# Optimization experiments

Hardware: AMD Instinct MI355X
Metric: run time of the kernel (lower is better)

Reference implementation:

```python
import jax, jax.numpy as jnp
import numpy as np


def setup_inputs() -> dict:
    key = jax.random.key(0)
    k1, k2 = jax.random.split(key)
    x = jax.random.normal(k1, (32, 128, 64, 64), dtype=jnp.float32)
    weight = jax.random.normal(k2, (256, 128, 3, 3), dtype=jnp.float32)
    return {"x": x, "weight": weight}


def reference(x, weight):
    # Batched VALID cross-correlation, stride 1 (same math as the triple loop
    # of single-channel conv2d calls summed over in_channels).
    # x: [B, Cin, H, W]; weight: [Cout, Cin, k, k] -> out: [B, Cout, H-k+1, W-k+1]
    return jax.lax.conv_general_dilated(
        x, weight,
        window_strides=(1, 1),
        padding="VALID",
        dimension_numbers=("NCHW", "OIHW", "NCHW"),
    )
```

## Files before the change

### kernel.cpp

```cpp
#include <hip/hip_runtime.h>


using bf16x8 = __attribute__((ext_vector_type(8))) __bf16;
using f32x4  = __attribute__((ext_vector_type(4))) float;

constexpr int CIN  = 128;
constexpr int HW   = 64;
constexpr int COUT = 256;
constexpr int OW   = 62;
constexpr int NS   = 62 * 62;
constexpr int NTOT = 32 * NS;
constexpr int KTOT = 9 * CIN;
constexpr int BM = 256, BN = 128, BK = 64;
constexpr int NT = KTOT / BK;

constexpr size_t AP_BYTES = (size_t)COUT * KTOT * 2;
constexpr size_t XP_BYTES = (size_t)32 * HW * HW * CIN * 2;
constexpr size_t WS_NEEDED = AP_BYTES + XP_BYTES;

constexpr int BUF_BYTES = 49152;
constexpr int BOFF_B    = 32768;

__device__ __forceinline__ unsigned short f2bf(float f) {
  unsigned u = __float_as_uint(f);
  u += 0x7fffu + ((u >> 16) & 1u);
  return (unsigned short)(u >> 16);
}
__device__ __forceinline__ unsigned pack2(float a, float b) {
  return (unsigned)f2bf(a) | ((unsigned)f2bf(b) << 16);
}

__device__ __forceinline__ void gld16(const void* g, void* l) {
  __builtin_amdgcn_global_load_lds(
      (const __attribute__((address_space(1))) unsigned int*)g,
      (__attribute__((address_space(3))) unsigned int*)l, 16, 0, 0);
}


__global__ __launch_bounds__(256)
void prepack_w(const float* __restrict__ w, unsigned* __restrict__ ap32) {
  const int idx = blockIdx.x * 256 + threadIdx.x;
  const int co  = idx / 576;
  const int k2  = idx - co * 576;
  const int k   = k2 * 2;
  const int tap = k >> 7;
  const int ci  = k & 127;
  const float v0 = w[(co * 128 + ci) * 9 + tap];
  const float v1 = w[(co * 128 + ci + 1) * 9 + tap];
  ap32[idx] = pack2(v0, v1);
}

__global__ __launch_bounds__(256)
void prepack_x(const float* __restrict__ x, unsigned* __restrict__ xp32) {
  const int bh = blockIdx.x;
  const int b  = bh >> 6, h = bh & 63;
  const int t  = threadIdx.x;
  const int c  = t & 63;
  const int w0 = (t >> 6) * 16;

  const float* p0 = x + (((size_t)(b * 128 + 2 * c) * HW) + h) * HW + w0;
  const float* p1 = p0 + (size_t)HW * HW;
  float r0[16], r1[16];
#pragma unroll
  for (int j = 0; j < 4; ++j) {
    *reinterpret_cast<float4*>(&r0[j * 4]) = reinterpret_cast<const float4*>(p0)[j];
    *reinterpret_cast<float4*>(&r1[j * 4]) = reinterpret_cast<const float4*>(p1)[j];
  }
  unsigned* o = xp32 + ((size_t)bh * HW + w0) * 64 + c;
#pragma unroll
  for (int j = 0; j < 16; ++j)
    o[j * 64] = pack2(r0[j], r1[j]);
}


__global__ __launch_bounds__(512, 2)
void conv_main(const unsigned short* __restrict__ Ap,
               const unsigned short* __restrict__ Xp,
               float* __restrict__ out) {
  __shared__ __align__(16) char lds[3 * BUF_BYTES];

  const int tid  = threadIdx.x;
  const int lane = tid & 63;
  const int wid  = tid >> 6;
  const int wm   = wid >> 1;
  const int wn   = wid & 1;
  const int n_base = blockIdx.x * BN;

  const int l3  = lane >> 3;
  const int sw8 = ((lane & 7) ^ l3) * 8;
  int aoff[4];
#pragma unroll
  for (int q = 0; q < 4; ++q) {
    const int r = (wid * 4 + q) * 8 + l3;
    aoff[q] = r * KTOT + sw8;
  }
  unsigned xoff[2];
#pragma unroll
  for (int q = 0; q < 2; ++q) {
    const int rn = (wid * 2 + q) * 8 + l3;
    const unsigned n  = n_base + rn;
    const unsigned bi = n / NS;
    const unsigned s0 = n - bi * NS;
    const unsigned oh = s0 / OW;
    const unsigned ww = s0 - oh * OW;
    xoff[q] = ((bi * HW + oh) * HW + ww) * CIN + sw8;
  }

  const int fr  = lane & 15;
  const int gl  = lane >> 4;
  const int f7  = fr & 7;
  const int sw0 = ((0 * 4 + gl) ^ f7) * 16;
  const int sw1 = ((1 * 4 + gl) ^ f7) * 16;
  const int arow = (wm * 64 + fr) * 128;
  const int brow = BOFF_B + (wn * 64 + fr) * 128;

  f32x4 acc[4][4] = {};

  auto STAGE = [&](int t, int buf) {
    const int tap   = t >> 1;
    const int kh    = tap / 3;
    const int kw    = tap - kh * 3;
    const int akoff = t * 64;
    const int xkoff = (kh * HW + kw) * CIN + (t & 1) * 64;
    char* lb = lds + buf * BUF_BYTES;
#pragma unroll
    for (int q = 0; q < 4; ++q)
      gld16(Ap + aoff[q] + akoff, lb + (wid * 4 + q) * 1024);
#pragma unroll
    for (int q = 0; q < 2; ++q)
      gld16(Xp + xoff[q] + xkoff, lb + BOFF_B + (wid * 2 + q) * 1024);
  };

  STAGE(0, 0);
  STAGE(1, 1);

#pragma unroll
  for (int t = 0; t < NT; ++t) {
    const int cb = t % 3;
    if (t < NT - 1) asm volatile("s_waitcnt vmcnt(6)" ::: "memory");
    else            asm volatile("s_waitcnt vmcnt(0)" ::: "memory");
    __builtin_amdgcn_s_barrier();
    __builtin_amdgcn_sched_barrier(0);

    const char* lb = lds + cb * BUF_BYTES;

    bf16x8 a0[4], b0[4];
#pragma unroll
    for (int mi = 0; mi < 4; ++mi)
      a0[mi] = *reinterpret_cast<const bf16x8*>(lb + arow + mi * 2048 + sw0);
#pragma unroll
    for (int ni = 0; ni < 4; ++ni)
      b0[ni] = *reinterpret_cast<const bf16x8*>(lb + brow + ni * 2048 + sw0);

    if (t < NT - 2) STAGE(t + 2, (t + 2) % 3);

    __builtin_amdgcn_s_setprio(1);
#pragma unroll
    for (int mi = 0; mi < 4; ++mi)
#pragma unroll
      for (int ni = 0; ni < 4; ++ni)
        acc[mi][ni] = __builtin_amdgcn_mfma_f32_16x16x32_bf16(a0[mi], b0[ni],
                                                              acc[mi][ni], 0, 0, 0);
    __builtin_amdgcn_s_setprio(0);

    bf16x8 a1[4], b1[4];
#pragma unroll
    for (int mi = 0; mi < 4; ++mi)
      a1[mi] = *reinterpret_cast<const bf16x8*>(lb + arow + mi * 2048 + sw1);
#pragma unroll
    for (int ni = 0; ni < 4; ++ni)
      b1[ni] = *reinterpret_cast<const bf16x8*>(lb + brow + ni * 2048 + sw1);

    __builtin_amdgcn_s_setprio(1);
#pragma unroll
    for (int mi = 0; mi < 4; ++mi)
#pragma unroll
      for (int ni = 0; ni < 4; ++ni)
        acc[mi][ni] = __builtin_amdgcn_mfma_f32_16x16x32_bf16(a1[mi], b1[ni],
                                                              acc[mi][ni], 0, 0, 0);
    __builtin_amdgcn_s_setprio(0);
  }

#pragma unroll
  for (int ni = 0; ni < 4; ++ni) {
    const unsigned n  = n_base + wn * 64 + ni * 16 + (lane & 15);
    const unsigned b2 = n / NS;
    const unsigned s2 = n - b2 * NS;
    float* op = out + (size_t)b2 * (COUT * NS) + s2
                    + (size_t)(wm * 64 + (lane >> 4) * 4) * NS;
#pragma unroll
    for (int mi = 0; mi < 4; ++mi)
#pragma unroll
      for (int r = 0; r < 4; ++r)
        op[(mi * 16 + r) * NS] = acc[mi][ni][r];
  }
}


__global__ __launch_bounds__(256)
void conv_fallback(const float* __restrict__ x, const float* __restrict__ w,
                   float* __restrict__ out) {
  __shared__ __align__(16) unsigned short As[128 * 32];
  __shared__ __align__(16) unsigned short Bs[128 * 32];

  const int t    = threadIdx.x;
  const int lane = t & 63;
  const int wid  = t >> 6;
  const int wm   = wid >> 1;
  const int wn   = wid & 1;
  const int co_base = blockIdx.x * 128;
  const int n_base  = blockIdx.y * 128;

  const int bn  = t & 127;
  const int bg0 = t >> 7;
  const unsigned n0   = n_base + bn;
  const unsigned bidx = n0 / NS;
  const unsigned s0   = n0 - bidx * NS;
  const unsigned oh   = s0 / OW;
  const unsigned ow   = s0 - oh * OW;
  const float* xb = x + (bidx * (CIN * HW * HW) + oh * HW + ow);

  const int am  = t & 127;
  const int ag0 = (t >> 7) * 2;
  const float* wb = w + (co_base + am) * KTOT;

  f32x4 acc[4][4] = {};

  for (int ks = 0; ks < 36; ++ks) {
    const int tap = ks >> 2;
    const int ci0 = (ks & 3) * 32;
    const int kh  = tap / 3;
    const int kw  = tap - kh * 3;
    const int xo  = kh * HW + kw;

    float av[2][8], bv[2][8];
#pragma unroll
    for (int gi = 0; gi < 2; ++gi) {
      const int g = ag0 + gi;
#pragma unroll
      for (int j = 0; j < 8; ++j)
        av[gi][j] = wb[(ci0 + g * 8 + j) * 9 + tap];
    }
#pragma unroll
    for (int gi = 0; gi < 2; ++gi) {
      const int g = bg0 + gi * 2;
#pragma unroll
      for (int j = 0; j < 8; ++j)
        bv[gi][j] = xb[xo + (ci0 + g * 8 + j) * (HW * HW)];
    }

    __syncthreads();

#pragma unroll
    for (int gi = 0; gi < 2; ++gi) {
      const int g = ag0 + gi;
      uint4 pv;
      pv.x = pack2(av[gi][0], av[gi][1]);
      pv.y = pack2(av[gi][2], av[gi][3]);
      pv.z = pack2(av[gi][4], av[gi][5]);
      pv.w = pack2(av[gi][6], av[gi][7]);
      *reinterpret_cast<uint4*>(&As[am * 32 + ((g ^ ((am >> 1) & 3)) << 3)]) = pv;
    }
#pragma unroll
    for (int gi = 0; gi < 2; ++gi) {
      const int g = bg0 + gi * 2;
      uint4 pv;
      pv.x = pack2(bv[gi][0], bv[gi][1]);
      pv.y = pack2(bv[gi][2], bv[gi][3]);
      pv.z = pack2(bv[gi][4], bv[gi][5]);
      pv.w = pack2(bv[gi][6], bv[gi][7]);
      *reinterpret_cast<uint4*>(&Bs[bn * 32 + ((g ^ ((bn >> 1) & 3)) << 3)]) = pv;
    }

    __syncthreads();

    bf16x8 af[4], bfr[4];
    const int g = lane >> 4;
#pragma unroll
    for (int mi = 0; mi < 4; ++mi) {
      const int m = wm * 64 + mi * 16 + (lane & 15);
      af[mi] = *reinterpret_cast<const bf16x8*>(&As[m * 32 + ((g ^ ((m >> 1) & 3)) << 3)]);
    }
#pragma unroll
    for (int ni = 0; ni < 4; ++ni) {
      const int nn = wn * 64 + ni * 16 + (lane & 15);
      bfr[ni] = *reinterpret_cast<const bf16x8*>(&Bs[nn * 32 + ((g ^ ((nn >> 1) & 3)) << 3)]);
    }
#pragma unroll
    for (int mi = 0; mi < 4; ++mi)
#pragma unroll
      for (int ni = 0; ni < 4; ++ni)
        acc[mi][ni] = __builtin_amdgcn_mfma_f32_16x16x32_bf16(af[mi], bfr[ni],
                                                              acc[mi][ni], 0, 0, 0);
  }

#pragma unroll
  for (int ni = 0; ni < 4; ++ni) {
    const unsigned n  = n_base + wn * 64 + ni * 16 + (lane & 15);
    const unsigned b2 = n / NS;
    const unsigned s2 = n - b2 * NS;
    float* op = out + (size_t)b2 * (COUT * NS) + s2
                    + (size_t)(co_base + wm * 64 + (lane >> 4) * 4) * NS;
#pragma unroll
    for (int mi = 0; mi < 4; ++mi)
#pragma unroll
      for (int r = 0; r < 4; ++r)
        op[(mi * 16 + r) * NS] = acc[mi][ni][r];
  }
}

extern "C" void kernel_launch(void* const* d_in, const int* in_sizes, int n_in,
                              void* d_out, int out_size, void* d_ws, size_t ws_size,
                              hipStream_t stream) {
  const float* x = (const float*)d_in[0];
  const float* w = (const float*)d_in[1];
  float* out = (float*)d_out;

  if (ws_size >= WS_NEEDED) {
    unsigned* ap32 = (unsigned*)d_ws;
    unsigned short* Ap = (unsigned short*)d_ws;
    unsigned short* Xp = (unsigned short*)((char*)d_ws + AP_BYTES);
    unsigned* xp32 = (unsigned*)Xp;
    prepack_w<<<576, 256, 0, stream>>>(w, ap32);
    prepack_x<<<32 * HW, 256, 0, stream>>>(x, xp32);
    conv_main<<<dim3(NTOT / BN), 512, 0, stream>>>(Ap, Xp, out);
  } else {
    conv_fallback<<<dim3(2, NTOT / 128), 256, 0, stream>>>(x, w, out);
  }
}
```

Measured before the change: 113.5 us.

## Enlarge conv GEMM tile to 256x256 with double-buffered split-phase MFMA schedule

Changes the main implicit-GEMM block tile from 256x128 to 256x256 outputs, so each wave computes 128x64 with 32 accumulators and the weight tile is reused across twice as many output pixels. The triple-buffered LDS pipeline becomes a double buffer of 64 KB per stage. Each K-step is split into four MFMA quarter-phases that interleave LDS fragment reads and global prefetch, separated by extra barriers. The grid is rounded up and tail rows are clamped on load and skipped on store. In exchange it uses more registers (likely one block per CU despite launch_bounds 2), has more barriers per step, and hides memory latency with only one stage of prefetch.

```diff
diff --git a/kernel.cpp b/kernel.cpp
--- a/kernel.cpp
+++ b/kernel.cpp
@@ -11,15 +11,16 @@
 constexpr int NS   = 62 * 62;
 constexpr int NTOT = 32 * NS;
 constexpr int KTOT = 9 * CIN;
-constexpr int BM = 256, BN = 128, BK = 64;
+constexpr int BM = 256, BN = 256, BK = 64;
 constexpr int NT = KTOT / BK;
+constexpr int NBLK = (NTOT + BN - 1) / BN;
 
 constexpr size_t AP_BYTES = (size_t)COUT * KTOT * 2;
 constexpr size_t XP_BYTES = (size_t)32 * HW * HW * CIN * 2;
 constexpr size_t WS_NEEDED = AP_BYTES + XP_BYTES;
 
-constexpr int BUF_BYTES = 49152;
-constexpr int BOFF_B    = 32768;
+constexpr int BUF  = 65536;
+constexpr int BOFF = 32768;
 
 __device__ __forceinline__ unsigned short f2bf(float f) {
   unsigned u = __float_as_uint(f);
@@ -77,119 +78,137 @@
 void conv_main(const unsigned short* __restrict__ Ap,
                const unsigned short* __restrict__ Xp,
                float* __restrict__ out) {
-  __shared__ __align__(16) char lds[3 * BUF_BYTES];
+  __shared__ __align__(16) char lds[2 * BUF];
 
   const int tid  = threadIdx.x;
   const int lane = tid & 63;
   const int wid  = tid >> 6;
-  const int wm   = wid >> 1;
-  const int wn   = wid & 1;
+  const int wm   = wid & 1;
+  const int wn   = wid >> 1;
   const int n_base = blockIdx.x * BN;
 
   const int l3  = lane >> 3;
   const int sw8 = ((lane & 7) ^ l3) * 8;
   int aoff[4];
-#pragma unroll
-  for (int q = 0; q < 4; ++q) {
-    const int r = (wid * 4 + q) * 8 + l3;
-    aoff[q] = r * KTOT + sw8;
-  }
-  unsigned xoff[2];
-#pragma unroll
-  for (int q = 0; q < 2; ++q) {
-    const int rn = (wid * 2 + q) * 8 + l3;
-    const unsigned n  = n_base + rn;
+  unsigned xoff[4];
+#pragma unroll
+  for (int j = 0; j < 4; ++j) {
+    const int r = j * 64 + wid * 8 + l3;
+    aoff[j] = r * KTOT + sw8;
+    unsigned n = n_base + r;
+    if (n >= NTOT) n = NTOT - 1;
     const unsigned bi = n / NS;
     const unsigned s0 = n - bi * NS;
     const unsigned oh = s0 / OW;
     const unsigned ww = s0 - oh * OW;
-    xoff[q] = ((bi * HW + oh) * HW + ww) * CIN + sw8;
-  }
-
-  const int fr  = lane & 15;
-  const int gl  = lane >> 4;
-  const int f7  = fr & 7;
-  const int sw0 = ((0 * 4 + gl) ^ f7) * 16;
-  const int sw1 = ((1 * 4 + gl) ^ f7) * 16;
-  const int arow = (wm * 64 + fr) * 128;
-  const int brow = BOFF_B + (wn * 64 + fr) * 128;
-
-  f32x4 acc[4][4] = {};
-
-  auto STAGE = [&](int t, int buf) {
-    const int tap   = t >> 1;
-    const int kh    = tap / 3;
-    const int kw    = tap - kh * 3;
-    const int akoff = t * 64;
-    const int xkoff = (kh * HW + kw) * CIN + (t & 1) * 64;
-    char* lb = lds + buf * BUF_BYTES;
-#pragma unroll
-    for (int q = 0; q < 4; ++q)
-      gld16(Ap + aoff[q] + akoff, lb + (wid * 4 + q) * 1024);
-#pragma unroll
-    for (int q = 0; q < 2; ++q)
-      gld16(Xp + xoff[q] + xkoff, lb + BOFF_B + (wid * 2 + q) * 1024);
-  };
-
-  STAGE(0, 0);
-  STAGE(1, 1);
+    xoff[j] = ((bi * HW + oh) * HW + ww) * CIN + sw8;
+  }
+
+  const int fr = lane & 15;
+  const int gl = lane >> 4;
+  const int s0b = ((gl)     ^ (fr & 7)) * 16;
+  const int s1b = ((4 + gl) ^ (fr & 7)) * 16;
+  const int abase = (wm * 128 + fr) * 128;
+  const int bbase = BOFF + (wn * 64 + fr) * 128;
+
+  f32x4 acc[8][4] = {};
+  bf16x8 aq[8];
+  bf16x8 b0q[4], b1q[4];
+
+  auto STAGE_A = [&](int tt, char* dst) {
+#pragma unroll
+    for (int j = 0; j < 4; ++j)
+      gld16(Ap + aoff[j] + tt * 64, dst + (j * 64 + wid * 8) * 128);
+  };
+  auto STAGE_B = [&](int tt, char* dst) {
+    const int tap = tt >> 1;
+    const int kh  = tap / 3;
+    const int kw  = tap - kh * 3;
+    const int xk  = (kh * HW + kw) * CIN + (tt & 1) * 64;
+#pragma unroll
+    for (int j = 0; j < 4; ++j)
+      gld16(Xp + xoff[j] + xk, dst + BOFF + (j * 64 + wid * 8) * 128);
+  };
+
+  auto LOAD_A = [&](const char* cur, int mq) {
+#pragma unroll
+    for (int mi = 0; mi < 4; ++mi) {
+      aq[mi * 2 + 0] = *reinterpret_cast<const bf16x8*>(cur + abase + mq * 8192 + mi * 2048 + s0b);
+      aq[mi * 2 + 1] = *reinterpret_cast<const bf16x8*>(cur + abase + mq * 8192 + mi * 2048 + s1b);
+    }
+  };
+  auto LOAD_B = [&](const char* cur, int nq, bf16x8* bq) {
+#pragma unroll
+    for (int ni = 0; ni < 2; ++ni) {
+      bq[ni * 2 + 0] = *reinterpret_cast<const bf16x8*>(cur + bbase + nq * 4096 + ni * 2048 + s0b);
+      bq[ni * 2 + 1] = *reinterpret_cast<const bf16x8*>(cur + bbase + nq * 4096 + ni * 2048 + s1b);
+    }
+  };
+  auto MFMA16 = [&](int mq, int nq, const bf16x8* bq) {
+    __builtin_amdgcn_s_setprio(1);
+#pragma unroll
+    for (int mi = 0; mi < 4; ++mi)
+#pragma unroll
+      for (int ni = 0; ni < 2; ++ni)
+#pragma unroll
+        for (int kk = 0; kk < 2; ++kk)
+          acc[mq * 4 + mi][nq * 2 + ni] = __builtin_amdgcn_mfma_f32_16x16x32_bf16(
+              aq[mi * 2 + kk], bq[ni * 2 + kk], acc[mq * 4 + mi][nq * 2 + ni], 0, 0, 0);
+    __builtin_amdgcn_s_setprio(0);
+  };
+
+  STAGE_A(0, lds);
+  STAGE_B(0, lds);
 
 #pragma unroll
   for (int t = 0; t < NT; ++t) {
-    const int cb = t % 3;
-    if (t < NT - 1) asm volatile("s_waitcnt vmcnt(6)" ::: "memory");
-    else            asm volatile("s_waitcnt vmcnt(0)" ::: "memory");
+    char* cur = lds + (t & 1) * BUF;
+    char* nxt = lds + ((t + 1) & 1) * BUF;
+
+    if (t < NT - 1) {
+      STAGE_A(t + 1, nxt);
+      asm volatile("s_waitcnt vmcnt(4)" ::: "memory");
+    } else {
+      asm volatile("s_waitcnt vmcnt(0)" ::: "memory");
+    }
     __builtin_amdgcn_s_barrier();
     __builtin_amdgcn_sched_barrier(0);
-
-    const char* lb = lds + cb * BUF_BYTES;
-
-    bf16x8 a0[4], b0[4];
-#pragma unroll
-    for (int mi = 0; mi < 4; ++mi)
-      a0[mi] = *reinterpret_cast<const bf16x8*>(lb + arow + mi * 2048 + sw0);
-#pragma unroll
-    for (int ni = 0; ni < 4; ++ni)
-      b0[ni] = *reinterpret_cast<const bf16x8*>(lb + brow + ni * 2048 + sw0);
-
-    if (t < NT - 2) STAGE(t + 2, (t + 2) % 3);
-
-    __builtin_amdgcn_s_setprio(1);
-#pragma unroll
-    for (int mi = 0; mi < 4; ++mi)
-#pragma unroll
-      for (int ni = 0; ni < 4; ++ni)
-        acc[mi][ni] = __builtin_amdgcn_mfma_f32_16x16x32_bf16(a0[mi], b0[ni],
-                                                              acc[mi][ni], 0, 0, 0);
-    __builtin_amdgcn_s_setprio(0);
-
-    bf16x8 a1[4], b1[4];
-#pragma unroll
-    for (int mi = 0; mi < 4; ++mi)
-      a1[mi] = *reinterpret_cast<const bf16x8*>(lb + arow + mi * 2048 + sw1);
-#pragma unroll
-    for (int ni = 0; ni < 4; ++ni)
-      b1[ni] = *reinterpret_cast<const bf16x8*>(lb + brow + ni * 2048 + sw1);
-
-    __builtin_amdgcn_s_setprio(1);
-#pragma unroll
-    for (int mi = 0; mi < 4; ++mi)
-#pragma unroll
-      for (int ni = 0; ni < 4; ++ni)
-        acc[mi][ni] = __builtin_amdgcn_mfma_f32_16x16x32_bf16(a1[mi], b1[ni],
-                                                              acc[mi][ni], 0, 0, 0);
-    __builtin_amdgcn_s_setprio(0);
+    LOAD_A(cur, 0);
+    LOAD_B(cur, 0, b0q);
+    asm volatile("s_waitcnt lgkmcnt(0)" ::: "memory");
+    __builtin_amdgcn_sched_barrier(0);
+    MFMA16(0, 0, b0q);
+    __builtin_amdgcn_s_barrier();
+
+    LOAD_B(cur, 1, b1q);
+    if (t < NT - 1) STAGE_B(t + 1, nxt);
+    __builtin_amdgcn_s_barrier();
+    asm volatile("s_waitcnt lgkmcnt(0)" ::: "memory");
+    __builtin_amdgcn_sched_barrier(0);
+    MFMA16(0, 1, b1q);
+    __builtin_amdgcn_s_barrier();
+
+    LOAD_A(cur, 1);
+    __builtin_amdgcn_s_barrier();
+    asm volatile("s_waitcnt lgkmcnt(0)" ::: "memory");
+    __builtin_amdgcn_sched_barrier(0);
+    MFMA16(1, 1, b1q);
+    __builtin_amdgcn_s_barrier();
+
+    MFMA16(1, 0, b0q);
+    __builtin_amdgcn_s_barrier();
   }
 
 #pragma unroll
   for (int ni = 0; ni < 4; ++ni) {
-    const unsigned n  = n_base + wn * 64 + ni * 16 + (lane & 15);
+    const unsigned n = n_base + wn * 64 + ni * 16 + fr;
+    if (n >= NTOT) continue;
     const unsigned b2 = n / NS;
     const unsigned s2 = n - b2 * NS;
     float* op = out + (size_t)b2 * (COUT * NS) + s2
-                    + (size_t)(wm * 64 + (lane >> 4) * 4) * NS;
-#pragma unroll
-    for (int mi = 0; mi < 4; ++mi)
+                    + (size_t)(wm * 128 + gl * 4) * NS;
+#pragma unroll
+    for (int mi = 0; mi < 8; ++mi)
 #pragma unroll
       for (int r = 0; r < 4; ++r)
         op[(mi * 16 + r) * NS] = acc[mi][ni][r];
@@ -323,7 +342,7 @@
     unsigned* xp32 = (unsigned*)Xp;
     prepack_w<<<576, 256, 0, stream>>>(w, ap32);
     prepack_x<<<32 * HW, 256, 0, stream>>>(x, xp32);
-    conv_main<<<dim3(NTOT / BN), 512, 0, stream>>>(Ap, Xp, out);
+    conv_main<<<dim3(NBLK), 512, 0, stream>>>(Ap, Xp, out);
   } else {
     conv_fallback<<<dim3(2, NTOT / 128), 256, 0, stream>>>(x, w, out);
   }
```

After: 121.4 us. 6.9% more time.

## Halve M tile, switch to 32x32 MFMA, double-buffer, add XCD-aware block remap

Applied to the files above, without the earlier changes.

The main conv GEMM kernel now uses 128x128 tiles with 256 threads instead of 256x128 with 512 threads, so the Cout dimension is split across two workgroups. It switches from 16x16x32 to 32x32x16 bf16 MFMA, and from a 3-stage to a 2-stage LDS pipeline that waits for all loads every iteration. It also adds an XCD-aware remapping of block IDs so adjacent tiles land on the same chiplet for L2 reuse. In exchange, the X tile is reloaded twice and the pipeline overlaps less (full vmcnt(0) waits, setprio removed), while occupancy and LDS use per block improve.

```diff
diff --git a/kernel.cpp b/kernel.cpp
--- a/kernel.cpp
+++ b/kernel.cpp
@@ -3,6 +3,7 @@
 
 using bf16x8 = __attribute__((ext_vector_type(8))) __bf16;
 using f32x4  = __attribute__((ext_vector_type(4))) float;
+using f32x16 = __attribute__((ext_vector_type(16))) float;
 
 constexpr int CIN  = 128;
 constexpr int HW   = 64;
@@ -11,15 +12,16 @@
 constexpr int NS   = 62 * 62;
 constexpr int NTOT = 32 * NS;
 constexpr int KTOT = 9 * CIN;
-constexpr int BM = 256, BN = 128, BK = 64;
+constexpr int BM = 128, BN = 128, BK = 64;
 constexpr int NT = KTOT / BK;
+constexpr int NWG = 2 * (NTOT / BN);
 
 constexpr size_t AP_BYTES = (size_t)COUT * KTOT * 2;
 constexpr size_t XP_BYTES = (size_t)32 * HW * HW * CIN * 2;
 constexpr size_t WS_NEEDED = AP_BYTES + XP_BYTES;
 
-constexpr int BUF_BYTES = 49152;
-constexpr int BOFF_B    = 32768;
+constexpr int BUF  = 32768;
+constexpr int BOFF = 16384;
 
 __device__ __forceinline__ unsigned short f2bf(float f) {
   unsigned u = __float_as_uint(f);
@@ -73,32 +75,37 @@
 }
 
 
-__global__ __launch_bounds__(512, 2)
+__global__ __launch_bounds__(256, 2)
 void conv_main(const unsigned short* __restrict__ Ap,
                const unsigned short* __restrict__ Xp,
                float* __restrict__ out) {
-  __shared__ __align__(16) char lds[3 * BUF_BYTES];
+  __shared__ __align__(16) char lds[2 * BUF];
 
   const int tid  = threadIdx.x;
   const int lane = tid & 63;
   const int wid  = tid >> 6;
   const int wm   = wid >> 1;
   const int wn   = wid & 1;
-  const int n_base = blockIdx.x * BN;
+
+  int wg;
+  {
+    const int f = blockIdx.x;
+    constexpr int q = NWG / 8, r = NWG % 8;
+    const int xc = f % 8, p = f / 8;
+    wg = (xc < r ? xc * (q + 1) : r * (q + 1) + (xc - r) * q) + p;
+  }
+  const int co_base = (wg & 1) * BM;
+  const int n_base  = (wg >> 1) * BN;
 
   const int l3  = lane >> 3;
   const int sw8 = ((lane & 7) ^ l3) * 8;
   int aoff[4];
+  unsigned xoff[4];
 #pragma unroll
   for (int q = 0; q < 4; ++q) {
-    const int r = (wid * 4 + q) * 8 + l3;
-    aoff[q] = r * KTOT + sw8;
-  }
-  unsigned xoff[2];
-#pragma unroll
-  for (int q = 0; q < 2; ++q) {
-    const int rn = (wid * 2 + q) * 8 + l3;
-    const unsigned n  = n_base + rn;
+    const int rr = wid * 32 + q * 8 + l3;
+    aoff[q] = (co_base + rr) * KTOT + sw8;
+    const unsigned n  = n_base + rr;
     const unsigned bi = n / NS;
     const unsigned s0 = n - bi * NS;
     const unsigned oh = s0 / OW;
@@ -106,94 +113,75 @@
     xoff[q] = ((bi * HW + oh) * HW + ww) * CIN + sw8;
   }
 
-  const int fr  = lane & 15;
-  const int gl  = lane >> 4;
-  const int f7  = fr & 7;
-  const int sw0 = ((0 * 4 + gl) ^ f7) * 16;
-  const int sw1 = ((1 * 4 + gl) ^ f7) * 16;
-  const int arow = (wm * 64 + fr) * 128;
-  const int brow = BOFF_B + (wn * 64 + fr) * 128;
-
-  f32x4 acc[4][4] = {};
-
-  auto STAGE = [&](int t, int buf) {
-    const int tap   = t >> 1;
-    const int kh    = tap / 3;
-    const int kw    = tap - kh * 3;
-    const int akoff = t * 64;
-    const int xkoff = (kh * HW + kw) * CIN + (t & 1) * 64;
-    char* lb = lds + buf * BUF_BYTES;
+  const int cl = lane & 31;
+  const int gl = lane >> 5;
+  int sA[4];
+#pragma unroll
+  for (int kf = 0; kf < 4; ++kf)
+    sA[kf] = ((kf * 2 + gl) ^ (lane & 7)) * 16;
+  const int abase = (wm * 64 + cl) * 128;
+  const int bbase = BOFF + (wn * 64 + cl) * 128;
+
+  f32x16 acc[2][2] = {};
+
+  auto STAGE = [&](int t, char* dst) {
+    const int tap = t >> 1;
+    const int kh  = tap / 3;
+    const int kw  = tap - kh * 3;
+    const int ak  = tap * CIN + (t & 1) * 64;
+    const int xk  = (kh * HW + kw) * CIN + (t & 1) * 64;
 #pragma unroll
     for (int q = 0; q < 4; ++q)
-      gld16(Ap + aoff[q] + akoff, lb + (wid * 4 + q) * 1024);
-#pragma unroll
-    for (int q = 0; q < 2; ++q)
-      gld16(Xp + xoff[q] + xkoff, lb + BOFF_B + (wid * 2 + q) * 1024);
+      gld16(Ap + aoff[q] + ak, dst + (wid * 32 + q * 8) * 128);
+#pragma unroll
+    for (int q = 0; q < 4; ++q)
+      gld16(Xp + xoff[q] + xk, dst + BOFF + (wid * 32 + q * 8) * 128);
   };
 
-  STAGE(0, 0);
-  STAGE(1, 1);
+  STAGE(0, lds);
 
 #pragma unroll
   for (int t = 0; t < NT; ++t) {
-    const int cb = t % 3;
-    if (t < NT - 1) asm volatile("s_waitcnt vmcnt(6)" ::: "memory");
-    else            asm volatile("s_waitcnt vmcnt(0)" ::: "memory");
+    const char* cur = lds + (t & 1) * BUF;
+    asm volatile("s_waitcnt vmcnt(0)" ::: "memory");
     __builtin_amdgcn_s_barrier();
-    __builtin_amdgcn_sched_barrier(0);
-
-    const char* lb = lds + cb * BUF_BYTES;
-
-    bf16x8 a0[4], b0[4];
-#pragma unroll
-    for (int mi = 0; mi < 4; ++mi)
-      a0[mi] = *reinterpret_cast<const bf16x8*>(lb + arow + mi * 2048 + sw0);
-#pragma unroll
-    for (int ni = 0; ni < 4; ++ni)
-      b0[ni] = *reinterpret_cast<const bf16x8*>(lb + brow + ni * 2048 + sw0);
-
-    if (t < NT - 2) STAGE(t + 2, (t + 2) % 3);
-
-    __builtin_amdgcn_s_setprio(1);
-#pragma unroll
-    for (int mi = 0; mi < 4; ++mi)
-#pragma unroll
-      for (int ni = 0; ni < 4; ++ni)
-        acc[mi][ni] = __builtin_amdgcn_mfma_f32_16x16x32_bf16(a0[mi], b0[ni],
-                                                              acc[mi][ni], 0, 0, 0);
-    __builtin_amdgcn_s_setprio(0);
-
-    bf16x8 a1[4], b1[4];
-#pragma unroll
-    for (int mi = 0; mi < 4; ++mi)
-      a1[mi] = *reinterpret_cast<const bf16x8*>(lb + arow + mi * 2048 + sw1);
-#pragma unroll
-    for (int ni = 0; ni < 4; ++ni)
-      b1[ni] = *reinterpret_cast<const bf16x8*>(lb + brow + ni * 2048 + sw1);
-
-    __builtin_amdgcn_s_setprio(1);
-#pragma unroll
-    for (int mi = 0; mi < 4; ++mi)
-#pragma unroll
-      for (int ni = 0; ni < 4; ++ni)
-        acc[mi][ni] = __builtin_amdgcn_mfma_f32_16x16x32_bf16(a1[mi], b1[ni],
-                                                              acc[mi][ni], 0, 0, 0);
-    __builtin_amdgcn_s_setprio(0);
-  }
-
-#pragma unroll
-  for (int ni = 0; ni < 4; ++ni) {
-    const unsigned n  = n_base + wn * 64 + ni * 16 + (lane & 15);
-    const unsigned b2 = n / NS;
-    const unsigned s2 = n - b2 * NS;
-    float* op = out + (size_t)b2 * (COUT * NS) + s2
-                    + (size_t)(wm * 64 + (lane >> 4) * 4) * NS;
-#pragma unroll
-    for (int mi = 0; mi < 4; ++mi)
-#pragma unroll
-      for (int r = 0; r < 4; ++r)
-        op[(mi * 16 + r) * NS] = acc[mi][ni][r];
-  }
+    if (t + 1 < NT) STAGE(t + 1, lds + ((t + 1) & 1) * BUF);
+
+    bf16x8 a[2][4], b[2][4];
+#pragma unroll
+    for (int mt = 0; mt < 2; ++mt)
+#pragma unroll
+      for (int kf = 0; kf < 4; ++kf)
+        a[mt][kf] = *reinterpret_cast<const bf16x8*>(cur + abase + mt * 4096 + sA[kf]);
+#pragma unroll
+    for (int nt = 0; nt < 2; ++nt)
+#pragma unroll
+      for (int kf = 0; kf < 4; ++kf)
+        b[nt][kf] = *reinterpret_cast<const bf16x8*>(cur + bbase + nt * 4096 + sA[kf]);
+
+#pragma unroll
+    for (int kf = 0; kf < 4; ++kf)
+#pragma unroll
+      for (int mt = 0; mt < 2; ++mt)
+#pragma unroll
+        for (int nt = 0; nt < 2; ++nt)
+          acc[mt][nt] = __builtin_amdgcn_mfma_f32_32x32x16_bf16(
+              a[mt][kf], b[nt][kf], acc[mt][nt], 0, 0, 0);
+  }
+
+#pragma unroll
+  for (int mt = 0; mt < 2; ++mt)
+#pragma unroll
+    for (int nt = 0; nt < 2; ++nt) {
+      const unsigned n  = n_base + wn * 64 + nt * 32 + cl;
+      const unsigned b2 = n / NS;
+      const unsigned s2 = n - b2 * NS;
+      float* op = out + (size_t)b2 * (COUT * NS) + s2
+                      + (size_t)(co_base + wm * 64 + mt * 32 + gl * 4) * NS;
+#pragma unroll
+      for (int r = 0; r < 16; ++r)
+        op[((r & 3) + 8 * (r >> 2)) * NS] = acc[mt][nt][r];
+    }
 }
 
 
@@ -323,7 +311,7 @@
     unsigned* xp32 = (unsigned*)Xp;
     prepack_w<<<576, 256, 0, stream>>>(w, ap32);
     prepack_x<<<32 * HW, 256, 0, stream>>>(x, xp32);
-    conv_main<<<dim3(NTOT / BN), 512, 0, stream>>>(Ap, Xp, out);
+    conv_main<<<dim3(NWG), 256, 0, stream>>>(Ap, Xp, out);
   } else {
     conv_fallback<<<dim3(2, NTOT / 128), 256, 0, stream>>>(x, w, out);
   }
```

Result: faster. 110.2 us (-2.9%).
